# Performance work log

Hardware: AMD Instinct MI355X
Metric: run time of the kernel (lower is better)

The kernel has to match this reference:

```python
import jax, jax.numpy as jnp
import numpy as np

L_BBOX, L_GIOU, L_OBJ, AUX_W = 5.0, 2.0, 1.0, 0.5
EPS = 1e-7


def _xyxy(b):
    # cxcywh -> xyxy
    return jnp.concatenate([b[..., :2] - b[..., 2:] * 0.5,
                            b[..., :2] + b[..., 2:] * 0.5], axis=-1)


def _giou(a, b):
    # a, b: [..., 4] xyxy (broadcastable) -> giou [...]
    area_a = (a[..., 2] - a[..., 0]) * (a[..., 3] - a[..., 1])
    area_b = (b[..., 2] - b[..., 0]) * (b[..., 3] - b[..., 1])
    lt = jnp.maximum(a[..., :2], b[..., :2])
    rb = jnp.minimum(a[..., 2:], b[..., 2:])
    wh = jnp.maximum(rb - lt, 0.0)
    inter = wh[..., 0] * wh[..., 1]
    union = area_a + area_b - inter
    iou = inter / (union + EPS)
    lte = jnp.minimum(a[..., :2], b[..., :2])
    rbe = jnp.maximum(a[..., 2:], b[..., 2:])
    whe = jnp.maximum(rbe - lte, 0.0)
    enc = whe[..., 0] * whe[..., 1]
    return iou - (enc - union) / (enc + EPS)


def _bce_sum(logits, targets):
    # numerically stable BCE-with-logits, reduction='sum'
    return jnp.sum(jnp.maximum(logits, 0.0) - logits * targets
                   + jnp.log1p(jnp.exp(-jnp.abs(logits))))


def _hungarian(cost):
    # exact Kuhn-Munkres (shortest augmenting path), rectangular, minimization
    cost = np.asarray(cost, dtype=np.float64)
    transposed = cost.shape[0] > cost.shape[1]
    if transposed:
        cost = cost.T
    n, m = cost.shape
    u = np.zeros(n + 1)
    v = np.zeros(m + 1)
    p = np.zeros(m + 1, dtype=np.int64)
    way = np.zeros(m + 1, dtype=np.int64)
    for i in range(1, n + 1):
        p[0] = i
        j0 = 0
        minv = np.full(m + 1, np.inf)
        used = np.zeros(m + 1, dtype=bool)
        while True:
            used[j0] = True
            i0 = p[j0]
            cur = cost[i0 - 1] - u[i0] - v[1:]
            free = ~used[1:]
            better = free & (cur < minv[1:])
            minv[1:] = np.where(better, cur, minv[1:])
            way[1:] = np.where(better, j0, way[1:])
            free_idx = np.nonzero(free)[0]
            jbest = free_idx[np.argmin(minv[1:][free_idx])]
            delta = minv[1 + jbest]
            u[p[used]] += delta
            v[used] -= delta
            minv[~used] -= delta
            j0 = jbest + 1
            if p[j0] == 0:
                break
        while j0:
            j1 = way[j0]
            p[j0] = p[j1]
            j0 = j1
    rows = p[1:] - 1
    cols = np.nonzero(rows >= 0)[0]
    rows = rows[cols]
    if transposed:
        rows, cols = cols, rows
    return rows.astype(np.int64), cols.astype(np.int64)


def _match(pred_bboxes, target_bboxes, bbox_mask):
    # batched cost matrix built on-device, Hungarian per sample (no_grad path)
    pxy = _xyxy(pred_bboxes)
    txy = _xyxy(target_bboxes)
    c_l1 = jnp.sum(jnp.abs(pred_bboxes[:, :, None, :] - target_bboxes[:, None, :, :]), -1)
    c_giou = -_giou(pxy[:, :, None, :], txy[:, None, :, :])
    C = np.asarray(L_BBOX * c_l1 + L_GIOU * c_giou)        # [B,N,M]
    mask = np.asarray(bbox_mask)
    B, N, M = C.shape
    pidx = np.zeros((B, M), np.int32)
    tidx = np.zeros((B, M), np.int32)
    pm = np.zeros((B, M), np.float32)
    for i in range(B):
        vid = np.nonzero(mask[i] > 0.5)[0]
        k = vid.size
        if k == 0:
            continue
        r, c = _hungarian(C[i][:, vid])
        pidx[i, :k] = r
        tidx[i, :k] = vid[c]
        pm[i, :k] = 1.0
    return jnp.asarray(pidx), jnp.asarray(tidx), jnp.asarray(pm)


def _det_losses(pred_bboxes, obj_logits, target_bboxes, pidx, tidx, pm):
    B, N = pred_bboxes.shape[:2]
    bi = jnp.arange(B)[:, None]
    mp = pred_bboxes[bi, pidx]               # [B,M,4] matched preds (padded)
    mt = target_bboxes[bi, tidx]             # [B,M,4] matched targets
    nb = jnp.maximum(pm.sum(), 1.0)
    bbox_loss = (jnp.abs(mp - mt).sum(-1) * pm).sum() / nb
    giou_loss = ((1.0 - _giou(_xyxy(mp), _xyxy(mt))) * pm).sum() / nb
    obj_t = jnp.zeros((B, N), pred_bboxes.dtype).at[bi, pidx].max(pm)
    obj_loss = _bce_sum(obj_logits[..., 0], obj_t) / (B * N)
    return bbox_loss, giou_loss, obj_loss, obj_t


def _total(cls_logits, label, pred_bboxes, obj_scores, target_bboxes,
           aux_pred_bboxes, aux_obj_scores, pidx, tidx, pm):
    B = cls_logits.shape[0]
    cls_loss = -jax.nn.log_softmax(cls_logits, -1)[jnp.arange(B), label].mean()
    bbox_loss, giou_loss, obj_loss, obj_t = _det_losses(
        pred_bboxes, obj_scores, target_bboxes, pidx, tidx, pm)
    # aux losses, vectorized over L decoder layers
    L = aux_pred_bboxes.shape[0]
    bi = jnp.arange(B)[:, None]
    mpa = aux_pred_bboxes[:, bi, pidx]                      # [L,B,M,4]
    mt = target_bboxes[bi, tidx][None]                      # [1,B,M,4]
    nb = jnp.maximum(pm.sum(), 1.0)
    aux_bbox = (jnp.abs(mpa - mt).sum(-1) * pm[None]).sum() / nb
    aux_giou = ((1.0 - _giou(_xyxy(mpa), _xyxy(mt))) * pm[None]).sum() / nb
    N = pred_bboxes.shape[1]
    aux_obj = _bce_sum(aux_obj_scores[..., 0], obj_t[None]) / (B * N)
    aux_loss = (L_BBOX * aux_bbox + L_GIOU * aux_giou + L_OBJ * aux_obj) * AUX_W / L
    return (cls_loss + L_BBOX * bbox_loss + L_GIOU * giou_loss
            + L_OBJ * obj_loss + aux_loss)


def setup_inputs() -> dict:
    B, N, M, L, C = 32, 300, 60, 5, 1000
    ks = jax.random.split(jax.random.key(0), 9)
    cls_logits = jax.random.normal(ks[0], (B, C), jnp.float32)
    label = jax.random.randint(ks[1], (B,), 0, C)
    pred_bboxes = jax.random.uniform(ks[2], (B, N, 4), jnp.float32)
    obj_scores = jax.random.normal(ks[3], (B, N, 1), jnp.float32)
    cxcy = jax.random.uniform(ks[4], (B, M, 2), jnp.float32, 0.2, 0.8)
    wh = jax.random.uniform(ks[5], (B, M, 2), jnp.float32, 0.05, 0.35)
    target_bboxes = jnp.concatenate([cxcy, wh], -1)
    counts = jax.random.randint(ks[6], (B,), 1, M + 1)
    bbox_mask = (jnp.arange(M)[None, :] < counts[:, None]).astype(jnp.float32)
    aux_pred_bboxes = jax.random.uniform(ks[7], (L, B, N, 4), jnp.float32)
    aux_obj_scores = jax.random.normal(ks[8], (L, B, N, 1), jnp.float32)
    return {"cls_logits": cls_logits, "label": label,
            "pred_bboxes": pred_bboxes, "obj_scores": obj_scores,
            "target_bboxes": target_bboxes, "bbox_mask": bbox_mask,
            "aux_pred_bboxes": aux_pred_bboxes,
            "aux_obj_scores": aux_obj_scores}


def reference(cls_logits, label, pred_bboxes, obj_scores, target_bboxes,
              bbox_mask, aux_pred_bboxes, aux_obj_scores):
    pidx, tidx, pm = _match(pred_bboxes, target_bboxes, bbox_mask)
    return _total(cls_logits, label, pred_bboxes, obj_scores, target_bboxes,
                  aux_pred_bboxes, aux_obj_scores, pidx, tidx, pm)
```

## Files before the change

### kernel.cpp

```cpp
#include <hip/hip_runtime.h>
#include <math.h>

#define BN   32
#define NN   300
#define MM   60
#define LAUX 5
#define CNUM 1000

#define LC_ROWS 54
#define CINF 3.0e38f

#define ACC_CLS   0
#define ACC_OBJ   1
#define ACC_AOBJ  2
#define ACC_BBOX  3
#define ACC_GIOU  4
#define ACC_ABBOX 5
#define ACC_AGIOU 6
#define ACC_NB    7

__device__ float  g_cost[BN * MM * NN + 64];
__device__ int    g_match[BN * NN];
__device__ double g_acc[8];

__device__ __forceinline__ float giou_box(float ax0, float ay0, float ax1, float ay1,
                                          float bx0, float by0, float bx1, float by1) {
    const float EPS = 1e-7f;
    float area_a = (ax1 - ax0) * (ay1 - ay0);
    float area_b = (bx1 - bx0) * (by1 - by0);
    float ltx = fmaxf(ax0, bx0), lty = fmaxf(ay0, by0);
    float rbx = fminf(ax1, bx1), rby = fminf(ay1, by1);
    float w = fmaxf(rbx - ltx, 0.0f), h = fmaxf(rby - lty, 0.0f);
    float inter = w * h;
    float uni = area_a + area_b - inter;
    float iou = inter / (uni + EPS);
    float ex0 = fminf(ax0, bx0), ey0 = fminf(ay0, by0);
    float ex1 = fmaxf(ax1, bx1), ey1 = fmaxf(ay1, by1);
    float ew = fmaxf(ex1 - ex0, 0.0f), eh = fmaxf(ey1 - ey0, 0.0f);
    float enc = ew * eh;
    return iou - (enc - uni) / (enc + EPS);
}

__global__ void cost_kernel(const float* __restrict__ pred, const float* __restrict__ tgt) {
    if (blockIdx.x == 0 && threadIdx.x < 8) g_acc[threadIdx.x] = 0.0;
    int idx = blockIdx.x * blockDim.x + threadIdx.x;
    if (idx >= BN * MM * NN) return;
    int n = idx % NN;
    int m = (idx / NN) % MM;
    int b = idx / (NN * MM);
    const float* p = pred + ((size_t)(b * NN + n)) * 4;
    const float* t = tgt + ((size_t)(b * MM + m)) * 4;
    float p0 = p[0], p1 = p[1], p2 = p[2], p3 = p[3];
    float t0 = t[0], t1 = t[1], t2 = t[2], t3 = t[3];
    float l1 = fabsf(p0 - t0) + fabsf(p1 - t1) + fabsf(p2 - t2) + fabsf(p3 - t3);
    float gi = giou_box(p0 - p2 * 0.5f, p1 - p3 * 0.5f, p0 + p2 * 0.5f, p1 + p3 * 0.5f,
                        t0 - t2 * 0.5f, t1 - t3 * 0.5f, t0 + t2 * 0.5f, t1 + t3 * 0.5f);
    g_cost[idx] = 5.0f * l1 - 2.0f * gi;
}


__device__ __forceinline__ unsigned enc_key(float x, int col) {
    unsigned u = __float_as_uint(x);
    unsigned e = (u & 0x80000000u) ? ~u : (u | 0x80000000u);
    return (e & 0xFFFFFE00u) | (unsigned)col;
}
__device__ __forceinline__ float dec_key(unsigned kk) {
    unsigned e = kk & 0xFFFFFE00u;
    unsigned u = (e & 0x80000000u) ? (e & 0x7FFFFFFFu) : ~e;
    return __uint_as_float(u);
}

__device__ __forceinline__ unsigned wave_min_u32(unsigned k) {
#define WSTEP(C) { unsigned t = (unsigned)__builtin_amdgcn_update_dpp((int)k, (int)k, (C), 0xF, 0xF, false); \
                   k = (t < k) ? t : k; }
    WSTEP(0x111) WSTEP(0x112) WSTEP(0x114) WSTEP(0x118) WSTEP(0x142) WSTEP(0x143)
#undef WSTEP
    return (unsigned)__builtin_amdgcn_readlane((int)k, 63);
}

__device__ __forceinline__ int sel5i(const int* a, int s) {
    int r = a[0];
    r = (s == 1) ? a[1] : r;
    r = (s == 2) ? a[2] : r;
    r = (s == 3) ? a[3] : r;
    r = (s == 4) ? a[4] : r;
    return r;
}
__device__ __forceinline__ float sel5f(const float* a, int s) {
    float r = a[0];
    r = (s == 1) ? a[1] : r;
    r = (s == 2) ? a[2] : r;
    r = (s == 3) ? a[3] : r;
    r = (s == 4) ? a[4] : r;
    return r;
}
__device__ __forceinline__ int rdlane_i(int x, int l) { return __builtin_amdgcn_readlane(x, l); }
__device__ __forceinline__ float rdlane_f(float x, int l) {
    return __uint_as_float((unsigned)__builtin_amdgcn_readlane(__float_as_int(x), l));
}

__global__ __launch_bounds__(64) void hung_kernel(const float* __restrict__ mask) {
    const int b = blockIdx.x;
    const int lane = threadIdx.x;
    __shared__ float lc[LC_ROWS * NN + 24];

    float mval = (lane < MM) ? mask[b * MM + lane] : 0.0f;
    int k = __popcll(__ballot(mval > 0.5f));

    const float* cb = g_cost + (size_t)b * (MM * NN);
    int stage = (k < LC_ROWS) ? k : LC_ROWS;
    int nf4 = stage * (NN / 4);
    for (int t = lane; t < nf4; t += 64) ((float4*)lc)[t] = ((const float4*)cb)[t];
    __syncthreads();

    float v[5], minv[5], uc[5];
    int pc[5], way[5];
    int used_inv = 0;
#pragma unroll
    for (int s = 0; s < 5; s++) {
        v[s] = 0.0f; uc[s] = 0.0f; pc[s] = 0; way[s] = 0; minv[s] = CINF;
        if (s * 64 + lane >= NN) used_inv |= 1 << s;
    }

    unsigned long long assigned = 0ull;
    float u_row = 0.0f;

    for (int r = 0; r < k; r++) {
        const float* rowp = (r < LC_ROWS) ? (lc + r * NN) : (cb + (size_t)r * NN);
        float rv[5];
#pragma unroll
        for (int s = 0; s < 5; s++) rv[s] = rowp[s * 64 + lane];
        unsigned kbest = 0xFFFFFFFFu;
#pragma unroll
        for (int s = 0; s < 5; s++) {
            int c = s * 64 + lane;
            unsigned kk = ((used_inv >> s) & 1) ? 0xFFFFFFFFu : enc_key(rv[s], c);
            kbest = (kk < kbest) ? kk : kbest;
        }
        unsigned kmin = wave_min_u32(kbest);
        float umin = dec_key(kmin);
        int jcol = (int)(kmin & 0x1FFu);
        if (lane == r) u_row = umin;
        int sl = jcol >> 6, ow = jcol & 63;
        int pj = rdlane_i(sel5i(pc, sl), ow);
        if (pj == 0) {
            if (lane == ow) {
                if      (sl == 0) { pc[0] = r + 1; uc[0] = umin; }
                else if (sl == 1) { pc[1] = r + 1; uc[1] = umin; }
                else if (sl == 2) { pc[2] = r + 1; uc[2] = umin; }
                else if (sl == 3) { pc[3] = r + 1; uc[3] = umin; }
                else              { pc[4] = r + 1; uc[4] = umin; }
            }
            assigned |= (1ull << r);
        }
    }

    for (int r = 0; r < k; r++) {
        if ((assigned >> r) & 1ull) continue;
        int used = used_inv;
#pragma unroll
        for (int s = 0; s < 5; s++) minv[s] = CINF;
        float u_cur = rdlane_f(u_row, r);
        float u_i0 = u_cur;
        int i0 = r + 1;
        int j0 = 0;

        for (int guard = 0; guard < NN + 4; guard++) {
            if (j0 > 0) {
                int c0 = j0 - 1;
                if (lane == (c0 & 63)) used |= 1 << (c0 >> 6);
            }
            const float* rowp = (i0 <= LC_ROWS) ? (lc + (i0 - 1) * NN)
                                                : (cb + (size_t)(i0 - 1) * NN);
            float rv[5];
#pragma unroll
            for (int s = 0; s < 5; s++) rv[s] = rowp[s * 64 + lane];
            unsigned kbest = 0xFFFFFFFFu;
#pragma unroll
            for (int s = 0; s < 5; s++) {
                int c = s * 64 + lane;
                bool skip = (used >> s) & 1;
                float cur = rv[s] - u_i0 - v[s];
                bool lt = !skip && (cur < minv[s]);
                minv[s] = lt ? cur : minv[s];
                way[s]  = lt ? j0 : way[s];
                unsigned kk = skip ? 0xFFFFFFFFu : enc_key(minv[s], c);
                kbest = (kk < kbest) ? kk : kbest;
            }
            unsigned kmin = wave_min_u32(kbest);
            float delta = dec_key(kmin);
            int jb = (int)(kmin & 0x1FFu);

            int sl = jb >> 6, ow = jb & 63;
            int pj = rdlane_i(sel5i(pc, sl), ow);
            float uj = rdlane_f(sel5f(uc, sl), ow);

            u_cur += delta;
#pragma unroll
            for (int s = 0; s < 5; s++) {
                bool us = (used >> s) & 1;
                v[s]    = us ? v[s] - delta   : v[s];
                uc[s]   = us ? uc[s] + delta  : uc[s];
                minv[s] = us ? minv[s]        : minv[s] - delta;
            }

            j0 = jb + 1;
            if (pj == 0) break;
            i0 = pj;
            u_i0 = uj;
        }

        int j = j0;
        int safety = 0;
        while (j && safety++ < NN + 4) {
            int co = j - 1, ow = co & 63, sl = co >> 6;
            int j1 = rdlane_i(sel5i(way, sl), ow);
            int pnew; float unew;
            if (j1 == 0) { pnew = r + 1; unew = u_cur; }
            else {
                int co1 = j1 - 1, ow1 = co1 & 63, sl1 = co1 >> 6;
                pnew = rdlane_i(sel5i(pc, sl1), ow1);
                unew = rdlane_f(sel5f(uc, sl1), ow1);
            }
            if (lane == ow) {
                if      (sl == 0) { pc[0] = pnew; uc[0] = unew; }
                else if (sl == 1) { pc[1] = pnew; uc[1] = unew; }
                else if (sl == 2) { pc[2] = pnew; uc[2] = unew; }
                else if (sl == 3) { pc[3] = pnew; uc[3] = unew; }
                else              { pc[4] = pnew; uc[4] = unew; }
            }
            j = j1;
        }
    }

#pragma unroll
    for (int s = 0; s < 5; s++) {
        int c = s * 64 + lane;
        if (c < NN) g_match[b * NN + c] = pc[s] - 1;
    }
}


__device__ __forceinline__ double bce_term(float x, float t) {
    return (double)(fmaxf(x, 0.0f) - x * t + log1pf(expf(-fabsf(x))));
}

#define PAIR_BLOCKS ((BN * NN + 255) / 256)

__global__ __launch_bounds__(256) void losses_kernel(
    const float* __restrict__ pred, const float* __restrict__ tgt,
    const float* __restrict__ auxp, const float* __restrict__ obj,
    const float* __restrict__ auxobj, const float* __restrict__ logits,
    const int* __restrict__ label)
{
    const int tid = threadIdx.x;
    const int blk = blockIdx.x;
    __shared__ float  smax[256];
    __shared__ double ssum[256];

    if (blk < PAIR_BLOCKS) {
        int idx = blk * 256 + tid;
        double sb = 0.0, sg = 0.0, sab = 0.0, sag = 0.0, nb = 0.0, so = 0.0, sao = 0.0;
        if (idx < BN * NN) {
            int t = g_match[idx];
            float tv = (t >= 0) ? 1.0f : 0.0f;
            so = bce_term(obj[idx], tv);
            for (int l = 0; l < LAUX; l++)
                sao += bce_term(auxobj[l * BN * NN + idx], tv);
            if (t >= 0) {
                int b = idx / NN;
                const float* p = pred + (size_t)idx * 4;
                const float* tg = tgt + ((size_t)(b * MM + t)) * 4;
                float t0 = tg[0], t1 = tg[1], t2 = tg[2], t3 = tg[3];
                float tx0 = t0 - t2 * 0.5f, ty0 = t1 - t3 * 0.5f;
                float tx1 = t0 + t2 * 0.5f, ty1 = t1 + t3 * 0.5f;
                {
                    float p0 = p[0], p1 = p[1], p2 = p[2], p3 = p[3];
                    float l1 = fabsf(p0 - t0) + fabsf(p1 - t1) + fabsf(p2 - t2) + fabsf(p3 - t3);
                    float gi = giou_box(p0 - p2 * 0.5f, p1 - p3 * 0.5f, p0 + p2 * 0.5f, p1 + p3 * 0.5f,
                                        tx0, ty0, tx1, ty1);
                    sb = (double)l1;
                    sg = (double)(1.0f - gi);
                    nb = 1.0;
                }
                for (int l = 0; l < LAUX; l++) {
                    const float* a = auxp + ((size_t)l * BN * NN + idx) * 4;
                    float a0 = a[0], a1 = a[1], a2 = a[2], a3 = a[3];
                    float l1 = fabsf(a0 - t0) + fabsf(a1 - t1) + fabsf(a2 - t2) + fabsf(a3 - t3);
                    float gi = giou_box(a0 - a2 * 0.5f, a1 - a3 * 0.5f, a0 + a2 * 0.5f, a1 + a3 * 0.5f,
                                        tx0, ty0, tx1, ty1);
                    sab += (double)l1;
                    sag += (double)(1.0f - gi);
                }
            }
        }
        for (int off = 32; off; off >>= 1) {
            sb  += __shfl_down(sb, off, 64);
            sg  += __shfl_down(sg, off, 64);
            sab += __shfl_down(sab, off, 64);
            sag += __shfl_down(sag, off, 64);
            nb  += __shfl_down(nb, off, 64);
            so  += __shfl_down(so, off, 64);
            sao += __shfl_down(sao, off, 64);
        }
        if ((tid & 63) == 0) {
            atomicAdd(&g_acc[ACC_BBOX], sb);
            atomicAdd(&g_acc[ACC_GIOU], sg);
            atomicAdd(&g_acc[ACC_ABBOX], sab);
            atomicAdd(&g_acc[ACC_AGIOU], sag);
            atomicAdd(&g_acc[ACC_NB], nb);
            atomicAdd(&g_acc[ACC_OBJ], so);
            atomicAdd(&g_acc[ACC_AOBJ], sao);
        }
    } else {
        const int b = blk - PAIR_BLOCKS;
        const float* row = logits + (size_t)b * CNUM;
        float mx = -1e30f;
        for (int c = tid; c < CNUM; c += 256) mx = fmaxf(mx, row[c]);
        smax[tid] = mx;
        __syncthreads();
        for (int s = 128; s; s >>= 1) {
            if (tid < s) smax[tid] = fmaxf(smax[tid], smax[tid + s]);
            __syncthreads();
        }
        mx = smax[0];
        double s = 0.0;
        for (int c = tid; c < CNUM; c += 256) s += exp((double)(row[c] - mx));
        ssum[tid] = s;
        __syncthreads();
        for (int st = 128; st; st >>= 1) {
            if (tid < st) ssum[tid] += ssum[tid + st];
            __syncthreads();
        }
        if (tid == 0) {
            double lse = log(ssum[0]) + (double)mx;
            atomicAdd(&g_acc[ACC_CLS], lse - (double)row[label[b]]);
        }
    }
}

__global__ void final_kernel(float* __restrict__ out) {
    if (threadIdx.x == 0 && blockIdx.x == 0) {
        double nb = g_acc[ACC_NB];
        if (nb < 1.0) nb = 1.0;
        double cls = g_acc[ACC_CLS] / (double)BN;
        double bbox = g_acc[ACC_BBOX] / nb;
        double giou = g_acc[ACC_GIOU] / nb;
        double obj = g_acc[ACC_OBJ] / (double)(BN * NN);
        double ab = g_acc[ACC_ABBOX] / nb;
        double ag = g_acc[ACC_AGIOU] / nb;
        double ao = g_acc[ACC_AOBJ] / (double)(BN * NN);
        double aux = (5.0 * ab + 2.0 * ag + 1.0 * ao) * 0.5 / (double)LAUX;
        out[0] = (float)(cls + 5.0 * bbox + 2.0 * giou + obj + aux);
    }
}

extern "C" void kernel_launch(void* const* d_in, const int* in_sizes, int n_in,
                              void* d_out, int out_size, void* d_ws, size_t ws_size,
                              hipStream_t stream) {
    const float* cls_logits = (const float*)d_in[0];
    const int* label = (const int*)d_in[1];
    const float* pred_bboxes = (const float*)d_in[2];
    const float* obj_scores = (const float*)d_in[3];
    const float* target_bboxes = (const float*)d_in[4];
    const float* bbox_mask = (const float*)d_in[5];
    const float* aux_pred = (const float*)d_in[6];
    const float* aux_obj = (const float*)d_in[7];
    float* out = (float*)d_out;

    cost_kernel<<<(BN * MM * NN + 255) / 256, 256, 0, stream>>>(pred_bboxes, target_bboxes);
    hung_kernel<<<BN, 64, 0, stream>>>(bbox_mask);
    losses_kernel<<<PAIR_BLOCKS + BN, 256, 0, stream>>>(pred_bboxes, target_bboxes, aux_pred,
                                                        obj_scores, aux_obj, cls_logits, label);
    final_kernel<<<1, 1, 0, stream>>>(out);
}
```

Baseline: 245.6 us.

## Fuse cost computation into Hungarian kernel and fold final reduction into losses

Removes the separate cost kernel and its global cost matrix. Each Hungarian block now computes its batch's cost rows directly into LDS using two waves, and keeps any rows past the LDS capacity in registers. The final scalar reduction moves into the losses kernel through a last-block-done counter, which cuts two launches. The Hungarian loop also prefetches the next row before the dual update and derives the initial row potential on the fly. In exchange it adds register pressure from the overflow rows and relies on an atomic completion counter.

```diff
diff --git a/kernel.cpp b/kernel.cpp
--- a/kernel.cpp
+++ b/kernel.cpp
@@ -8,6 +8,7 @@
 #define CNUM 1000
 
 #define LC_ROWS 54
+#define REX_ROWS 6
 #define CINF 3.0e38f
 
 #define ACC_CLS   0
@@ -19,9 +20,12 @@
 #define ACC_AGIOU 6
 #define ACC_NB    7
 
-__device__ float  g_cost[BN * MM * NN + 64];
+#define PAIR_BLOCKS ((BN * NN + 255) / 256)
+#define GRID_L (PAIR_BLOCKS + BN)
+
 __device__ int    g_match[BN * NN];
 __device__ double g_acc[8];
+__device__ int    g_done;
 
 __device__ __forceinline__ float giou_box(float ax0, float ay0, float ax1, float ay1,
                                           float bx0, float by0, float bx1, float by1) {
@@ -41,23 +45,12 @@
     return iou - (enc - uni) / (enc + EPS);
 }
 
-__global__ void cost_kernel(const float* __restrict__ pred, const float* __restrict__ tgt) {
-    if (blockIdx.x == 0 && threadIdx.x < 8) g_acc[threadIdx.x] = 0.0;
-    int idx = blockIdx.x * blockDim.x + threadIdx.x;
-    if (idx >= BN * MM * NN) return;
-    int n = idx % NN;
-    int m = (idx / NN) % MM;
-    int b = idx / (NN * MM);
-    const float* p = pred + ((size_t)(b * NN + n)) * 4;
-    const float* t = tgt + ((size_t)(b * MM + m)) * 4;
-    float p0 = p[0], p1 = p[1], p2 = p[2], p3 = p[3];
-    float t0 = t[0], t1 = t[1], t2 = t[2], t3 = t[3];
-    float l1 = fabsf(p0 - t0) + fabsf(p1 - t1) + fabsf(p2 - t2) + fabsf(p3 - t3);
-    float gi = giou_box(p0 - p2 * 0.5f, p1 - p3 * 0.5f, p0 + p2 * 0.5f, p1 + p3 * 0.5f,
-                        t0 - t2 * 0.5f, t1 - t3 * 0.5f, t0 + t2 * 0.5f, t1 + t3 * 0.5f);
-    g_cost[idx] = 5.0f * l1 - 2.0f * gi;
-}
-
+__device__ __forceinline__ float cost_pt(float4 p, float4 t) {
+    float l1 = fabsf(p.x - t.x) + fabsf(p.y - t.y) + fabsf(p.z - t.z) + fabsf(p.w - t.w);
+    float gi = giou_box(p.x - p.z * 0.5f, p.y - p.w * 0.5f, p.x + p.z * 0.5f, p.y + p.w * 0.5f,
+                        t.x - t.z * 0.5f, t.y - t.w * 0.5f, t.x + t.z * 0.5f, t.y + t.w * 0.5f);
+    return 5.0f * l1 - 2.0f * gi;
+}
 
 __device__ __forceinline__ unsigned enc_key(float x, int col) {
     unsigned u = __float_as_uint(x);
@@ -99,48 +92,97 @@
     return __uint_as_float((unsigned)__builtin_amdgcn_readlane(__float_as_int(x), l));
 }
 
-__global__ __launch_bounds__(64) void hung_kernel(const float* __restrict__ mask) {
+__global__ __launch_bounds__(128) void hung_kernel(const float* __restrict__ pred,
+                                                   const float* __restrict__ tgt,
+                                                   const float* __restrict__ mask) {
     const int b = blockIdx.x;
-    const int lane = threadIdx.x;
-    __shared__ float lc[LC_ROWS * NN + 24];
+    const int tid = threadIdx.x;
+    const int lane = tid & 63;
+    const int wid = tid >> 6;
+
+    __shared__ float lc[LC_ROWS * NN + 32];
+
+    if (b == 0 && tid == 0) {
+        __hip_atomic_store(&g_done, 0, __ATOMIC_RELAXED, __HIP_MEMORY_SCOPE_AGENT);
+#pragma unroll
+        for (int i = 0; i < 8; i++)
+            __hip_atomic_store(&g_acc[i], 0.0, __ATOMIC_RELAXED, __HIP_MEMORY_SCOPE_AGENT);
+    }
 
     float mval = (lane < MM) ? mask[b * MM + lane] : 0.0f;
     int k = __popcll(__ballot(mval > 0.5f));
 
-    const float* cb = g_cost + (size_t)b * (MM * NN);
-    int stage = (k < LC_ROWS) ? k : LC_ROWS;
-    int nf4 = stage * (NN / 4);
-    for (int t = lane; t < nf4; t += 64) ((float4*)lc)[t] = ((const float4*)cb)[t];
-    __syncthreads();
-
-    float v[5], minv[5], uc[5];
-    int pc[5], way[5];
-    int used_inv = 0;
+    float4 pb[5];
 #pragma unroll
     for (int s = 0; s < 5; s++) {
-        v[s] = 0.0f; uc[s] = 0.0f; pc[s] = 0; way[s] = 0; minv[s] = CINF;
-        if (s * 64 + lane >= NN) used_inv |= 1 << s;
-    }
-
-    unsigned long long assigned = 0ull;
-    float u_row = 0.0f;
-
-    for (int r = 0; r < k; r++) {
-        const float* rowp = (r < LC_ROWS) ? (lc + r * NN) : (cb + (size_t)r * NN);
-        float rv[5];
-#pragma unroll
-        for (int s = 0; s < 5; s++) rv[s] = rowp[s * 64 + lane];
-        unsigned kbest = 0xFFFFFFFFu;
+        int c = s * 64 + lane;
+        pb[s] = (c < NN) ? ((const float4*)pred)[b * NN + c]
+                         : make_float4(0.f, 0.f, 0.f, 0.f);
+    }
+
+    float rex[REX_ROWS][5];
+
+    int kl = (k < LC_ROWS) ? k : LC_ROWS;
+    for (int r = wid; r < kl; r += 2) {
+        float4 tb = ((const float4*)tgt)[b * MM + r];
 #pragma unroll
         for (int s = 0; s < 5; s++) {
             int c = s * 64 + lane;
-            unsigned kk = ((used_inv >> s) & 1) ? 0xFFFFFFFFu : enc_key(rv[s], c);
-            kbest = (kk < kbest) ? kk : kbest;
+            if (c < NN) lc[r * NN + c] = cost_pt(pb[s], tb);
+        }
+    }
+    if (wid == 0) {
+        for (int r = LC_ROWS; r < k; r++) {
+            float4 tb = ((const float4*)tgt)[b * MM + r];
+#pragma unroll
+            for (int s = 0; s < 5; s++) rex[r - LC_ROWS][s] = cost_pt(pb[s], tb);
+        }
+    }
+    __syncthreads();
+    if (wid == 1) return;
+
+#define LOAD_ROW(ROW, RV) do {                                                  \
+    int _r = (ROW);                                                             \
+    if (_r < LC_ROWS) {                                                         \
+        _Pragma("unroll")                                                       \
+        for (int _s = 0; _s < 5; _s++) RV[_s] = lc[_r * NN + _s * 64 + lane];   \
+    } else {                                                                    \
+        switch (_r - LC_ROWS) {                                                 \
+        case 0: _Pragma("unroll") for (int _s = 0; _s < 5; _s++) RV[_s] = rex[0][_s]; break; \
+        case 1: _Pragma("unroll") for (int _s = 0; _s < 5; _s++) RV[_s] = rex[1][_s]; break; \
+        case 2: _Pragma("unroll") for (int _s = 0; _s < 5; _s++) RV[_s] = rex[2][_s]; break; \
+        case 3: _Pragma("unroll") for (int _s = 0; _s < 5; _s++) RV[_s] = rex[3][_s]; break; \
+        case 4: _Pragma("unroll") for (int _s = 0; _s < 5; _s++) RV[_s] = rex[4][_s]; break; \
+        default: _Pragma("unroll") for (int _s = 0; _s < 5; _s++) RV[_s] = rex[5][_s]; break; \
+        }                                                                       \
+    }                                                                           \
+} while (0)
+
+    int used_inv = 0;
+#pragma unroll
+    for (int s = 0; s < 5; s++)
+        if (s * 64 + lane >= NN) used_inv |= 1 << s;
+
+    float v[5], uc[5], minv[5];
+    int pc[5], way[5];
+#pragma unroll
+    for (int s = 0; s < 5; s++) { v[s] = 0.0f; uc[s] = 0.0f; pc[s] = 0; way[s] = 0; }
+
+    unsigned long long freeM = 0ull;
+    for (int r = 0; r < k; r++) {
+        float rv[5];
+        LOAD_ROW(r, rv);
+        unsigned kbest = 0xFFFFFFFFu;
+#pragma unroll
+        for (int s = 0; s < 5; s++) {
+            if (!((used_inv >> s) & 1)) {
+                unsigned kk = enc_key(rv[s], s * 64 + lane);
+                kbest = (kk < kbest) ? kk : kbest;
+            }
         }
         unsigned kmin = wave_min_u32(kbest);
         float umin = dec_key(kmin);
         int jcol = (int)(kmin & 0x1FFu);
-        if (lane == r) u_row = umin;
         int sl = jcol >> 6, ow = jcol & 63;
         int pj = rdlane_i(sel5i(pc, sl), ow);
         if (pj == 0) {
@@ -151,18 +193,28 @@
                 else if (sl == 3) { pc[3] = r + 1; uc[3] = umin; }
                 else              { pc[4] = r + 1; uc[4] = umin; }
             }
-            assigned |= (1ull << r);
-        }
-    }
-
-    for (int r = 0; r < k; r++) {
-        if ((assigned >> r) & 1ull) continue;
+        } else {
+            freeM |= 1ull << r;
+        }
+    }
+
+    while (freeM) {
+        int r = (int)__builtin_ctzll(freeM);
+        freeM &= freeM - 1;
+
         int used = used_inv;
 #pragma unroll
         for (int s = 0; s < 5; s++) minv[s] = CINF;
-        float u_cur = rdlane_f(u_row, r);
+
+        float rv[5];
+        LOAD_ROW(r, rv);
+        unsigned kb0 = 0xFFFFFFFFu;
+#pragma unroll
+        for (int s = 0; s < 5; s++)
+            if (!((used_inv >> s) & 1))
+                { unsigned kk = enc_key(rv[s] - v[s], s * 64 + lane); kb0 = (kk < kb0) ? kk : kb0; }
+        float u_cur = dec_key(wave_min_u32(kb0));
         float u_i0 = u_cur;
-        int i0 = r + 1;
         int j0 = 0;
 
         for (int guard = 0; guard < NN + 4; guard++) {
@@ -170,11 +222,6 @@
                 int c0 = j0 - 1;
                 if (lane == (c0 & 63)) used |= 1 << (c0 >> 6);
             }
-            const float* rowp = (i0 <= LC_ROWS) ? (lc + (i0 - 1) * NN)
-                                                : (cb + (size_t)(i0 - 1) * NN);
-            float rv[5];
-#pragma unroll
-            for (int s = 0; s < 5; s++) rv[s] = rowp[s * 64 + lane];
             unsigned kbest = 0xFFFFFFFFu;
 #pragma unroll
             for (int s = 0; s < 5; s++) {
@@ -195,19 +242,23 @@
             int pj = rdlane_i(sel5i(pc, sl), ow);
             float uj = rdlane_f(sel5f(uc, sl), ow);
 
+            float rvn[5];
+            if (pj > 0) LOAD_ROW(pj - 1, rvn);
+
             u_cur += delta;
 #pragma unroll
             for (int s = 0; s < 5; s++) {
                 bool us = (used >> s) & 1;
-                v[s]    = us ? v[s] - delta   : v[s];
-                uc[s]   = us ? uc[s] + delta  : uc[s];
-                minv[s] = us ? minv[s]        : minv[s] - delta;
+                v[s]    = us ? v[s] - delta  : v[s];
+                uc[s]   = us ? uc[s] + delta : uc[s];
+                minv[s] = us ? minv[s]       : minv[s] - delta;
             }
 
             j0 = jb + 1;
             if (pj == 0) break;
-            i0 = pj;
             u_i0 = uj;
+#pragma unroll
+            for (int s = 0; s < 5; s++) rv[s] = rvn[s];
         }
 
         int j = j0;
@@ -238,20 +289,19 @@
         int c = s * 64 + lane;
         if (c < NN) g_match[b * NN + c] = pc[s] - 1;
     }
+#undef LOAD_ROW
 }
 
 
 __device__ __forceinline__ double bce_term(float x, float t) {
     return (double)(fmaxf(x, 0.0f) - x * t + log1pf(expf(-fabsf(x))));
 }
-
-#define PAIR_BLOCKS ((BN * NN + 255) / 256)
 
 __global__ __launch_bounds__(256) void losses_kernel(
     const float* __restrict__ pred, const float* __restrict__ tgt,
     const float* __restrict__ auxp, const float* __restrict__ obj,
     const float* __restrict__ auxobj, const float* __restrict__ logits,
-    const int* __restrict__ label)
+    const int* __restrict__ label, float* __restrict__ out)
 {
     const int tid = threadIdx.x;
     const int blk = blockIdx.x;
@@ -269,25 +319,22 @@
                 sao += bce_term(auxobj[l * BN * NN + idx], tv);
             if (t >= 0) {
                 int b = idx / NN;
-                const float* p = pred + (size_t)idx * 4;
-                const float* tg = tgt + ((size_t)(b * MM + t)) * 4;
-                float t0 = tg[0], t1 = tg[1], t2 = tg[2], t3 = tg[3];
-                float tx0 = t0 - t2 * 0.5f, ty0 = t1 - t3 * 0.5f;
-                float tx1 = t0 + t2 * 0.5f, ty1 = t1 + t3 * 0.5f;
+                float4 p = ((const float4*)pred)[idx];
+                float4 tg = ((const float4*)tgt)[b * MM + t];
+                float tx0 = tg.x - tg.z * 0.5f, ty0 = tg.y - tg.w * 0.5f;
+                float tx1 = tg.x + tg.z * 0.5f, ty1 = tg.y + tg.w * 0.5f;
                 {
-                    float p0 = p[0], p1 = p[1], p2 = p[2], p3 = p[3];
-                    float l1 = fabsf(p0 - t0) + fabsf(p1 - t1) + fabsf(p2 - t2) + fabsf(p3 - t3);
-                    float gi = giou_box(p0 - p2 * 0.5f, p1 - p3 * 0.5f, p0 + p2 * 0.5f, p1 + p3 * 0.5f,
+                    float l1 = fabsf(p.x - tg.x) + fabsf(p.y - tg.y) + fabsf(p.z - tg.z) + fabsf(p.w - tg.w);
+                    float gi = giou_box(p.x - p.z * 0.5f, p.y - p.w * 0.5f, p.x + p.z * 0.5f, p.y + p.w * 0.5f,
                                         tx0, ty0, tx1, ty1);
                     sb = (double)l1;
                     sg = (double)(1.0f - gi);
                     nb = 1.0;
                 }
                 for (int l = 0; l < LAUX; l++) {
-                    const float* a = auxp + ((size_t)l * BN * NN + idx) * 4;
-                    float a0 = a[0], a1 = a[1], a2 = a[2], a3 = a[3];
-                    float l1 = fabsf(a0 - t0) + fabsf(a1 - t1) + fabsf(a2 - t2) + fabsf(a3 - t3);
-                    float gi = giou_box(a0 - a2 * 0.5f, a1 - a3 * 0.5f, a0 + a2 * 0.5f, a1 + a3 * 0.5f,
+                    float4 a = ((const float4*)auxp)[(size_t)l * BN * NN + idx];
+                    float l1 = fabsf(a.x - tg.x) + fabsf(a.y - tg.y) + fabsf(a.z - tg.z) + fabsf(a.w - tg.w);
+                    float gi = giou_box(a.x - a.z * 0.5f, a.y - a.w * 0.5f, a.x + a.z * 0.5f, a.y + a.w * 0.5f,
                                         tx0, ty0, tx1, ty1);
                     sab += (double)l1;
                     sag += (double)(1.0f - gi);
@@ -337,21 +384,27 @@
             atomicAdd(&g_acc[ACC_CLS], lse - (double)row[label[b]]);
         }
     }
-}
-
-__global__ void final_kernel(float* __restrict__ out) {
-    if (threadIdx.x == 0 && blockIdx.x == 0) {
-        double nb = g_acc[ACC_NB];
-        if (nb < 1.0) nb = 1.0;
-        double cls = g_acc[ACC_CLS] / (double)BN;
-        double bbox = g_acc[ACC_BBOX] / nb;
-        double giou = g_acc[ACC_GIOU] / nb;
-        double obj = g_acc[ACC_OBJ] / (double)(BN * NN);
-        double ab = g_acc[ACC_ABBOX] / nb;
-        double ag = g_acc[ACC_AGIOU] / nb;
-        double ao = g_acc[ACC_AOBJ] / (double)(BN * NN);
-        double aux = (5.0 * ab + 2.0 * ag + 1.0 * ao) * 0.5 / (double)LAUX;
-        out[0] = (float)(cls + 5.0 * bbox + 2.0 * giou + obj + aux);
+
+    __syncthreads();
+    if (tid == 0) {
+        __threadfence();
+        int done = atomicAdd(&g_done, 1);
+        if (done == GRID_L - 1) {
+            __threadfence();
+            double a[8];
+#pragma unroll
+            for (int i = 0; i < 8; i++) a[i] = atomicAdd(&g_acc[i], 0.0);
+            double nb = a[ACC_NB] < 1.0 ? 1.0 : a[ACC_NB];
+            double cls  = a[ACC_CLS] / (double)BN;
+            double bbox = a[ACC_BBOX] / nb;
+            double giou = a[ACC_GIOU] / nb;
+            double objl = a[ACC_OBJ] / (double)(BN * NN);
+            double ab   = a[ACC_ABBOX] / nb;
+            double ag   = a[ACC_AGIOU] / nb;
+            double ao   = a[ACC_AOBJ] / (double)(BN * NN);
+            double aux  = (5.0 * ab + 2.0 * ag + 1.0 * ao) * 0.5 / (double)LAUX;
+            out[0] = (float)(cls + 5.0 * bbox + 2.0 * giou + objl + aux);
+        }
     }
 }
 
@@ -368,9 +421,7 @@
     const float* aux_obj = (const float*)d_in[7];
     float* out = (float*)d_out;
 
-    cost_kernel<<<(BN * MM * NN + 255) / 256, 256, 0, stream>>>(pred_bboxes, target_bboxes);
-    hung_kernel<<<BN, 64, 0, stream>>>(bbox_mask);
-    losses_kernel<<<PAIR_BLOCKS + BN, 256, 0, stream>>>(pred_bboxes, target_bboxes, aux_pred,
-                                                        obj_scores, aux_obj, cls_logits, label);
-    final_kernel<<<1, 1, 0, stream>>>(out);
-}
+    hung_kernel<<<BN, 128, 0, stream>>>(pred_bboxes, target_bboxes, bbox_mask);
+    losses_kernel<<<GRID_L, 256, 0, stream>>>(pred_bboxes, target_bboxes, aux_pred,
+                                              obj_scores, aux_obj, cls_logits, label, out);
+}
```

Result: slower. 335.9 us (+36.8%).
